# Performance work log

Hardware: AMD Instinct MI355X
Metric: run time of the kernel (lower is better)

The kernel has to match this reference:

```python
import jax, jax.numpy as jnp
import numpy as np
from jax import lax

N = 100000
E = 1600000
LAG = 50
H = 32          # hid_dim = in_channels = out_channels
FEA = 4
OUT = 1


def setup_inputs() -> dict:
    key = jax.random.key(0)
    ks = jax.random.split(key, 16)
    inp = {
        "node_x": jax.random.normal(ks[0], (N, FEA), jnp.float32),
        "node_yx": jax.random.normal(ks[1], (N, LAG), jnp.float32),
        "edge_index": jax.random.randint(ks[2], (2, E), 0, N, jnp.int64),
        "edge_weight": jax.random.uniform(ks[3], (E,), jnp.float32),
        # LSTM params (torch gate order: i, f, g, o)
        "w_ih": jax.random.normal(ks[4], (4 * H, 1), jnp.float32) * 0.1,
        "w_hh": jax.random.normal(ks[5], (4 * H, H), jnp.float32) * 0.1,
        "b_ih": jnp.zeros((4 * H,), jnp.float32),
        "b_hh": jnp.zeros((4 * H,), jnp.float32),
        # time attention
        "att_W": jax.random.normal(ks[6], (LAG, H), jnp.float32) * 0.1,
        # fc after attention pooling
        "fc_W": jax.random.normal(ks[7], (H, H), jnp.float32) * 0.1,
        "fc_b": jnp.zeros((H,), jnp.float32),
        # GCN layers
        "gcn1_W": jax.random.normal(ks[8], (H, H), jnp.float32) * 0.1,
        "gcn1_b": jnp.zeros((H,), jnp.float32),
        "gcn2_W": jax.random.normal(ks[9], (H, H), jnp.float32) * 0.1,
        "gcn2_b": jnp.zeros((H,), jnp.float32),
        # final linear
        "lin_W": jax.random.normal(ks[10], (H + FEA, OUT), jnp.float32) * 0.1,
        "lin_b": jnp.zeros((OUT,), jnp.float32),
    }
    return inp


def _lstm(x, w_ih, w_hh, b_ih, b_hh):
    # x: [N, T, in_dim]; returns ht: [N, T, H]
    n, t, _ = x.shape
    h = w_hh.shape[1]
    xp = jnp.einsum('nti,gi->ntg', x, w_ih) + b_ih  # [N,T,4H], precompute input proj
    xp = jnp.swapaxes(xp, 0, 1)                      # [T,N,4H]

    def step(carry, xt):
        hprev, cprev = carry
        g = xt + hprev @ w_hh.T + b_hh               # [N,4H]
        i = jax.nn.sigmoid(g[:, 0 * h:1 * h])
        f = jax.nn.sigmoid(g[:, 1 * h:2 * h])
        gg = jnp.tanh(g[:, 2 * h:3 * h])
        o = jax.nn.sigmoid(g[:, 3 * h:4 * h])
        c = f * cprev + i * gg
        hnew = o * jnp.tanh(c)
        return (hnew, c), hnew

    init = (jnp.zeros((n, h), x.dtype), jnp.zeros((n, h), x.dtype))
    _, hs = lax.scan(step, init, xp)
    return jnp.swapaxes(hs, 0, 1)                    # [N,T,H]


def _gcn(x, edge_index, edge_weight, W, b, num_nodes):
    # PyG GCNConv: x' = D^-1/2 (A + I) D^-1/2 (x W) + b
    xw = x @ W
    src = jnp.concatenate([edge_index[0], jnp.arange(num_nodes, dtype=edge_index.dtype)])
    dst = jnp.concatenate([edge_index[1], jnp.arange(num_nodes, dtype=edge_index.dtype)])
    ew = jnp.concatenate([edge_weight, jnp.ones((num_nodes,), edge_weight.dtype)])
    deg = jax.ops.segment_sum(ew, dst, num_segments=num_nodes)
    dis = jnp.where(deg > 0, deg ** -0.5, 0.0)
    norm = dis[src] * ew * dis[dst]                  # [E+N]
    msg = norm[:, None] * xw[src]                    # gather + scale
    out = jax.ops.segment_sum(msg, dst, num_segments=num_nodes)  # scatter-add
    return out + b


def reference(node_x, node_yx, edge_index, edge_weight,
              w_ih, w_hh, b_ih, b_hh, att_W, fc_W, fc_b,
              gcn1_W, gcn1_b, gcn2_W, gcn2_b, lin_W, lin_b):
    # ATT_LSTM
    ht = _lstm(node_yx[:, :, None], w_ih, w_hh, b_ih, b_hh)   # [N,LAG,H]
    scores = jnp.sum(ht * att_W, axis=2)                      # [N,LAG]
    att = jax.nn.softmax(scores, axis=1)
    pooled = jnp.einsum('nt,nth->nh', att, ht)                # [N,H]
    x1 = jax.nn.relu(pooled @ fc_W + fc_b)                    # [N,H]
    # dropout treated as identity (deterministic reference / eval mode)
    x2 = _gcn(x1, edge_index, edge_weight, gcn1_W, gcn1_b, N)
    x2 = _gcn(x2, edge_index, edge_weight, gcn2_W, gcn2_b, N)
    xcom = jnp.concatenate([x2, node_x], axis=1)              # [N,H+FEA]
    pred = jax.nn.relu(xcom @ lin_W + lin_b)                  # [N,1]
    return pred.squeeze(-1)                                   # [N]
```

## Files before the change

kernel.cpp:

```cpp
#include <hip/hip_runtime.h>
#include <hip/hip_bf16.h>
#include <stdint.h>
#include <math.h>

#define H 32
#define LAGN 50

typedef float f32x4 __attribute__((ext_vector_type(4)));
typedef short bf16x8 __attribute__((ext_vector_type(8)));

__device__ __forceinline__ float rcp_(float x){ return __builtin_amdgcn_rcpf(x); }
__device__ __forceinline__ float sigmoidf_(float x){ return rcp_(1.0f + __expf(-x)); }
__device__ __forceinline__ float tanhf_(float x){ return 1.0f - 2.0f*rcp_(__expf(2.0f*x) + 1.0f); }

__device__ __forceinline__ unsigned pk_bf2(float f0, float f1){
  union { __hip_bfloat162 b; unsigned u; } cv;
  cv.b = __float22bfloat162_rn(make_float2(f0, f1));
  return cv.u;
}
__device__ __forceinline__ void cvt8v(f32x4 a, f32x4 b, bf16x8& hi, bf16x8& lo){
  union U { bf16x8 v; unsigned d[4]; } Hu, Lu;
  #pragma unroll
  for (int p=0;p<2;p++){
    float f0=a[2*p], f1=a[2*p+1];
    unsigned uh = pk_bf2(f0,f1);
    float h0 = __uint_as_float(uh<<16);
    float h1 = __uint_as_float(uh & 0xffff0000u);
    Hu.d[p] = uh;  Lu.d[p] = pk_bf2(f0-h0, f1-h1);
    float g0=b[2*p], g1=b[2*p+1];
    unsigned ug = pk_bf2(g0,g1);
    float k0 = __uint_as_float(ug<<16);
    float k1 = __uint_as_float(ug & 0xffff0000u);
    Hu.d[2+p] = ug;  Lu.d[2+p] = pk_bf2(g0-k0, g1-k1);
  }
  hi = Hu.v; lo = Lu.v;
}

__global__ __launch_bounds__(256, 2) void k_lstm(
    const float* __restrict__ yx,
    const float* __restrict__ w_ih,
    const float* __restrict__ w_hh,
    const float* __restrict__ b_ih,
    const float* __restrict__ b_hh,
    const float* __restrict__ att_W,
    const float* __restrict__ fc_W,
    const float* __restrict__ fc_b,
    float* __restrict__ x1,
    int N)
{
  __shared__ float hs[4][16*36];
  const int wv = threadIdx.x >> 6;
  const int l  = threadIdx.x & 63;
  const int q  = l >> 4;
  const int cl = l & 15;
  const int nb = blockIdx.x*64 + wv*16;
  float* HS = hs[wv];

  bf16x8 Bhi[8], Blo[8];
  #pragma unroll
  for (int T=0; T<8; ++T){
    const float* p = w_hh + (size_t)(16*T + cl)*H + 8*q;
    f32x4 w0 = *(const f32x4*)p;
    f32x4 w1 = *(const f32x4*)(p+4);
    cvt8v(w0, w1, Bhi[T], Blo[T]);
  }

  float wihv[8], bsv[8];
  #pragma unroll
  for (int T=0;T<8;T++){
    int colg = 16*T + cl;
    wihv[T] = w_ih[colg];
    bsv[T]  = b_ih[colg] + b_hh[colg];
  }

  for (int i=l; i<16*36; i+=64) HS[i] = 0.f;

  float cst[4][2], Sv[4][2], Zv[4];
  #pragma unroll
  for (int idx=0;idx<4;idx++){
    Zv[idx]=0.f; cst[idx][0]=0.f; cst[idx][1]=0.f; Sv[idx][0]=0.f; Sv[idx][1]=0.f;
  }

  const int rr = nb + 4*q;
  const float* yp0 = yx + (size_t)(rr+0<N?rr+0:N-1)*LAGN;
  const float* yp1 = yx + (size_t)(rr+1<N?rr+1:N-1)*LAGN;
  const float* yp2 = yx + (size_t)(rr+2<N?rr+2:N-1)*LAGN;
  const float* yp3 = yx + (size_t)(rr+3<N?rr+3:N-1)*LAGN;

  #pragma unroll 1
  for (int t=0;t<LAGN;t++){
    float xtv[4] = {yp0[t], yp1[t], yp2[t], yp3[t]};
    float at0 = att_W[t*H + cl];
    float at1 = att_W[t*H + cl + 16];

    f32x4 a0 = *(const f32x4*)&HS[36*cl + 8*q];
    f32x4 a1 = *(const f32x4*)&HS[36*cl + 8*q + 4];
    bf16x8 Ahi, Alo;
    cvt8v(a0, a1, Ahi, Alo);

    f32x4 C[8];
    #pragma unroll
    for (int T=0;T<8;T++){
      f32x4 z;
      #pragma unroll
      for (int idx=0;idx<4;idx++) z[idx] = __builtin_fmaf(xtv[idx], wihv[T], bsv[T]);
      z = __builtin_amdgcn_mfma_f32_16x16x32_bf16(Ahi, Blo[T], z, 0,0,0);
      z = __builtin_amdgcn_mfma_f32_16x16x32_bf16(Alo, Bhi[T], z, 0,0,0);
      z = __builtin_amdgcn_mfma_f32_16x16x32_bf16(Ahi, Bhi[T], z, 0,0,0);
      C[T] = z;
    }

    float stp[4], hv[4][2];
    #pragma unroll
    for (int idx=0; idx<4; ++idx){
      stp[idx] = 0.f;
      #pragma unroll
      for (int jh=0; jh<2; ++jh){
        float iv = sigmoidf_(C[jh][idx]);
        float fv = sigmoidf_(C[2+jh][idx]);
        float gv = tanhf_(C[4+jh][idx]);
        float ov = sigmoidf_(C[6+jh][idx]);
        float cn = fv*cst[idx][jh] + iv*gv;
        cst[idx][jh] = cn;
        float hh = ov*tanhf_(cn);
        hv[idx][jh] = hh;
        stp[idx] += hh * (jh ? at1 : at0);
        HS[36*(4*q+idx) + cl + 16*jh] = hh;
      }
    }

    #pragma unroll
    for (int mask=1; mask<16; mask<<=1){
      #pragma unroll
      for (int idx=0;idx<4;idx++)
        stp[idx] += __shfl_xor(stp[idx], mask);
    }

    #pragma unroll
    for (int idx=0;idx<4;idx++){
      float pex = __expf(stp[idx]);
      Zv[idx] += pex;
      Sv[idx][0] += pex*hv[idx][0];
      Sv[idx][1] += pex*hv[idx][1];
    }
  }

  #pragma unroll
  for (int idx=0;idx<4;idx++){
    float iz = rcp_(Zv[idx]);
    HS[36*(4*q+idx) + cl]      = Sv[idx][0]*iz;
    HS[36*(4*q+idx) + cl + 16] = Sv[idx][1]*iz;
  }
  f32x4 p0 = *(const f32x4*)&HS[36*cl + 8*q];
  f32x4 p1 = *(const f32x4*)&HS[36*cl + 8*q + 4];
  bf16x8 Phi, Plo;
  cvt8v(p0, p1, Phi, Plo);

  #pragma unroll
  for (int T=0;T<2;T++){
    f32x4 w0, w1;
    #pragma unroll
    for (int i=0;i<4;i++){
      w0[i] = fc_W[(size_t)(8*q+i)*H + 16*T + cl];
      w1[i] = fc_W[(size_t)(8*q+4+i)*H + 16*T + cl];
    }
    bf16x8 Fhi, Flo;
    cvt8v(w0, w1, Fhi, Flo);
    float fcbv = fc_b[16*T + cl];
    f32x4 z = {fcbv, fcbv, fcbv, fcbv};
    z = __builtin_amdgcn_mfma_f32_16x16x32_bf16(Phi, Flo, z, 0,0,0);
    z = __builtin_amdgcn_mfma_f32_16x16x32_bf16(Plo, Fhi, z, 0,0,0);
    z = __builtin_amdgcn_mfma_f32_16x16x32_bf16(Phi, Fhi, z, 0,0,0);
    #pragma unroll
    for (int idx=0;idx<4;idx++){
      int r = nb + 4*q + idx;
      if (r < N) x1[(size_t)r*H + 16*T + cl] = fmaxf(z[idx], 0.f);
    }
  }
}

__global__ void k_deg_init(float* __restrict__ deg, int* __restrict__ cnt, int N){
  int i = blockIdx.x*blockDim.x + threadIdx.x;
  if (i < N){ deg[i] = 1.0f; cnt[i] = 0; }
}

__global__ void k_deg_cnt(const int* __restrict__ ei, const float* __restrict__ ew,
                          float* __restrict__ deg, int* __restrict__ cnt, int E){
  int e = blockIdx.x*blockDim.x + threadIdx.x;
  if (e < E){
    int d = ei[E+e];
    atomicAdd(&deg[d], ew[e]);
    atomicAdd(&cnt[d], 1);
  }
}

__global__ void k_dis(float* __restrict__ deg, int N){
  int i = blockIdx.x*blockDim.x + threadIdx.x;
  if (i < N) deg[i] = __frcp_rn(sqrtf(deg[i]));
}

__global__ __launch_bounds__(256) void k_scan1(const int* __restrict__ cnt,
                                               int* __restrict__ bsum, int N){
  __shared__ int wsm[4];
  int b = blockIdx.x, t = threadIdx.x;
  int base = b*1024 + t*4;
  int s = 0;
  #pragma unroll
  for (int i=0;i<4;i++) if (base+i < N) s += cnt[base+i];
  #pragma unroll
  for (int off=1; off<64; off<<=1) s += __shfl_xor(s, off);
  if ((t&63) == 0) wsm[t>>6] = s;
  __syncthreads();
  if (t == 0) bsum[b] = wsm[0]+wsm[1]+wsm[2]+wsm[3];
}

__global__ __launch_bounds__(64) void k_scan2(int* __restrict__ bsum, int nb){
  int lane = threadIdx.x;
  int carry = 0;
  for (int base=0; base<nb; base+=64){
    int i = base + lane;
    int v = (i<nb) ? bsum[i] : 0;
    int s = v;
    #pragma unroll
    for (int off=1; off<64; off<<=1){ int tt=__shfl_up(s,off); if (lane>=off) s+=tt; }
    if (i<nb) bsum[i] = carry + s - v;
    carry += __shfl(s, 63);
  }
}

__global__ __launch_bounds__(256) void k_scan3(int* cp,
                                               const int* __restrict__ bsum,
                                               int* __restrict__ rowptr, int N){
  __shared__ int wsm[4];
  int b = blockIdx.x, t = threadIdx.x, lane = t&63, w = t>>6;
  int base = b*1024 + t*4;
  int v[4];
  #pragma unroll
  for (int i=0;i<4;i++) v[i] = (base+i<N) ? cp[base+i] : 0;
  int tsum = v[0]+v[1]+v[2]+v[3];
  int s = tsum;
  #pragma unroll
  for (int off=1; off<64; off<<=1){ int tt=__shfl_up(s,off); if (lane>=off) s+=tt; }
  if (lane==63) wsm[w] = s;
  __syncthreads();
  int woff = 0;
  #pragma unroll
  for (int k=0;k<4;k++) if (k<w) woff += wsm[k];
  int e = bsum[b] + woff + (s - tsum);
  #pragma unroll
  for (int i=0;i<4;i++){
    if (base+i < N){ rowptr[base+i] = e; cp[base+i] = e; }
    if (base+i == N-1) rowptr[N] = e + v[i];
    e += v[i];
  }
}

__global__ void k_fill(const int* __restrict__ ei, const float* __restrict__ ew,
                       const float* __restrict__ dis, int* __restrict__ pos,
                       int2* __restrict__ cedge, int E){
  int e = blockIdx.x*blockDim.x + threadIdx.x;
  if (e < E){
    int s = ei[e], d = ei[E+e];
    int slot = atomicAdd(&pos[d], 1);
    cedge[slot] = make_int2(s, __float_as_int(dis[s]*ew[e]*dis[d]));
  }
}

__global__ __launch_bounds__(256) void k_xw(
    const float* __restrict__ x, const float* __restrict__ W,
    const float* __restrict__ b, const float* __restrict__ dis,
    float* __restrict__ xw, float* __restrict__ out, int N)
{
  int n = blockIdx.x*blockDim.x + threadIdx.x;
  if (n >= N) return;
  float xv[H];
  const float4* xr = (const float4*)(x + (size_t)n*H);
  #pragma unroll
  for (int q=0;q<H/4;q++){
    float4 v = xr[q];
    xv[4*q+0]=v.x; xv[4*q+1]=v.y; xv[4*q+2]=v.z; xv[4*q+3]=v.w;
  }
  float d = dis[n];
  float sn = d*d;
  float* xwr = xw + (size_t)n*H;
  float* outr = out + (size_t)n*H;
  #pragma unroll
  for (int j=0;j<H;j++){
    float a = 0.f;
    #pragma unroll
    for (int k=0;k<H;k++) a += xv[k]*W[k*H+j];
    xwr[j]  = a;
    outr[j] = sn*a + b[j];
  }
}

__global__ __launch_bounds__(256) void k_gather(
    const int* __restrict__ rowptr, const int2* __restrict__ cedge,
    const float* __restrict__ xw, float* __restrict__ out, int N)
{
  int wid = (int)((blockIdx.x*256u + threadIdx.x) >> 6);
  if (wid >= N) return;
  int lane = threadIdx.x & 63;
  int ch = lane & 31;
  int eh = lane >> 5;
  int start = rowptr[wid], end = rowptr[wid+1];
  float acc = 0.f;
  for (int j = start + eh; j < end; j += 2){
    int2 e = cedge[j];
    acc += __int_as_float(e.y) * xw[(size_t)e.x*H + ch];
  }
  acc += __shfl_xor(acc, 32);
  if (eh == 0){
    float* o = out + (size_t)wid*H + ch;
    *o += acc;
  }
}

__global__ void k_final(const float* __restrict__ x2, const float* __restrict__ nx,
                        const float* __restrict__ lw, const float* __restrict__ lb,
                        float* __restrict__ out, int N)
{
  int n = blockIdx.x*blockDim.x + threadIdx.x;
  if (n >= N) return;
  float a = lb[0];
  const float* xr = x2 + (size_t)n*H;
  #pragma unroll
  for (int j=0;j<H;j++) a += xr[j]*lw[j];
  const float* nr = nx + (size_t)n*4;
  #pragma unroll
  for (int f=0;f<4;f++) a += nr[f]*lw[H+f];
  out[n] = fmaxf(a, 0.f);
}

extern "C" void kernel_launch(void* const* d_in, const int* in_sizes, int n_in,
                              void* d_out, int out_size, void* d_ws, size_t ws_size,
                              hipStream_t stream) {
  const float* node_x   = (const float*)d_in[0];
  const float* node_yx  = (const float*)d_in[1];
  const int*   edge_idx = (const int*)  d_in[2];
  const float* edge_w   = (const float*)d_in[3];
  const float* w_ih     = (const float*)d_in[4];
  const float* w_hh     = (const float*)d_in[5];
  const float* b_ih     = (const float*)d_in[6];
  const float* b_hh     = (const float*)d_in[7];
  const float* att_W    = (const float*)d_in[8];
  const float* fc_W     = (const float*)d_in[9];
  const float* fc_b     = (const float*)d_in[10];
  const float* gcn1_W   = (const float*)d_in[11];
  const float* gcn1_b   = (const float*)d_in[12];
  const float* gcn2_W   = (const float*)d_in[13];
  const float* gcn2_b   = (const float*)d_in[14];
  const float* lin_W    = (const float*)d_in[15];
  const float* lin_b    = (const float*)d_in[16];
  float* out = (float*)d_out;

  int N = in_sizes[0] / 4;
  int E = in_sizes[3];

  float* ws = (float*)d_ws;
  float* x1     = ws;
  float* xw     = x1  + (size_t)N*H;
  float* o1     = xw  + (size_t)N*H;
  float* deg    = o1  + (size_t)N*H;
  int*   rowptr = (int*)(deg + N);
  int*   pos    = rowptr + (N+1);
  uintptr_t ca  = ((uintptr_t)(pos + N) + 7) & ~(uintptr_t)7;
  int2*  cedge  = (int2*)ca;
  int*   bsum   = (int*)(cedge + E);

  dim3 blk(256);
  int gN  = (N + 255) / 256;
  int gE  = (E + 255) / 256;
  int gL  = (N + 63) / 64;
  int gG  = (N + 3) / 4;
  int gS  = (N + 1023) / 1024;

  k_lstm<<<gL, blk, 0, stream>>>(node_yx, w_ih, w_hh, b_ih, b_hh,
                                 att_W, fc_W, fc_b, x1, N);
  k_deg_init<<<gN, blk, 0, stream>>>(deg, pos, N);
  k_deg_cnt <<<gE, blk, 0, stream>>>(edge_idx, edge_w, deg, pos, E);
  k_dis     <<<gN, blk, 0, stream>>>(deg, N);
  k_scan1   <<<gS, blk, 0, stream>>>(pos, bsum, N);
  k_scan2   <<<1, dim3(64), 0, stream>>>(bsum, gS);
  k_scan3   <<<gS, blk, 0, stream>>>(pos, bsum, rowptr, N);
  k_fill    <<<gE, blk, 0, stream>>>(edge_idx, edge_w, deg, pos, cedge, E);
  k_xw    <<<gN, blk, 0, stream>>>(x1, gcn1_W, gcn1_b, deg, xw, o1, N);
  k_gather<<<gG, blk, 0, stream>>>(rowptr, cedge, xw, o1, N);
  k_xw    <<<gN, blk, 0, stream>>>(o1, gcn2_W, gcn2_b, deg, xw, x1, N);
  k_gather<<<gG, blk, 0, stream>>>(rowptr, cedge, xw, x1, N);
  k_final<<<gN, blk, 0, stream>>>(x1, node_x, lin_W, lin_b, out, N);
}
```

Baseline: 772.9 us.

## Interleave two independent node tiles per wave in the LSTM kernel

```diff
diff --git a/kernel.cpp b/kernel.cpp
--- a/kernel.cpp
+++ b/kernel.cpp
@@ -36,6 +36,55 @@
   hi = Hu.v; lo = Lu.v;
 }
 
+struct C8 { f32x4 v[8]; };
+
+__device__ __forceinline__ C8 tile_mfma(
+    const float* HS, const bf16x8 (&Bhi)[8], const bf16x8 (&Blo)[8],
+    const float (&wihv)[8], const float (&bsv)[8], const float (&xtv)[4],
+    int q, int cl)
+{
+  f32x4 a0 = *(const f32x4*)&HS[36*cl + 8*q];
+  f32x4 a1 = *(const f32x4*)&HS[36*cl + 8*q + 4];
+  bf16x8 Ahi, Alo;
+  cvt8v(a0, a1, Ahi, Alo);
+  C8 C;
+  #pragma unroll
+  for (int T=0;T<8;T++){
+    f32x4 z;
+    #pragma unroll
+    for (int idx=0;idx<4;idx++) z[idx] = __builtin_fmaf(xtv[idx], wihv[T], bsv[T]);
+    z = __builtin_amdgcn_mfma_f32_16x16x32_bf16(Ahi, Blo[T], z, 0,0,0);
+    z = __builtin_amdgcn_mfma_f32_16x16x32_bf16(Alo, Bhi[T], z, 0,0,0);
+    z = __builtin_amdgcn_mfma_f32_16x16x32_bf16(Ahi, Bhi[T], z, 0,0,0);
+    C.v[T] = z;
+  }
+  return C;
+}
+
+__device__ __forceinline__ void tile_gates(
+    float* HS, const C8& C, float at0, float at1,
+    float (&cst)[4][2], float (&hv)[4][2], float (&stp)[4],
+    int q, int cl)
+{
+  #pragma unroll
+  for (int idx=0; idx<4; ++idx){
+    stp[idx] = 0.f;
+    #pragma unroll
+    for (int jh=0; jh<2; ++jh){
+      float iv = sigmoidf_(C.v[jh][idx]);
+      float fv = sigmoidf_(C.v[2+jh][idx]);
+      float gv = tanhf_(C.v[4+jh][idx]);
+      float ov = sigmoidf_(C.v[6+jh][idx]);
+      float cn = fv*cst[idx][jh] + iv*gv;
+      cst[idx][jh] = cn;
+      float hh = ov*tanhf_(cn);
+      hv[idx][jh] = hh;
+      stp[idx] += hh * (jh ? at1 : at0);
+      HS[36*(4*q+idx) + cl + 16*jh] = hh;
+    }
+  }
+}
+
 __global__ __launch_bounds__(256, 2) void k_lstm(
     const float* __restrict__ yx,
     const float* __restrict__ w_ih,
@@ -48,13 +97,15 @@
     float* __restrict__ x1,
     int N)
 {
-  __shared__ float hs[4][16*36];
+  __shared__ float hs[8][16*36];
   const int wv = threadIdx.x >> 6;
   const int l  = threadIdx.x & 63;
   const int q  = l >> 4;
   const int cl = l & 15;
-  const int nb = blockIdx.x*64 + wv*16;
-  float* HS = hs[wv];
+  const int nbA = blockIdx.x*128 + wv*32;
+  const int nbB = nbA + 16;
+  float* HSA = hs[2*wv];
+  float* HSB = hs[2*wv+1];
 
   bf16x8 Bhi[8], Blo[8];
   #pragma unroll
@@ -73,108 +124,98 @@
     bsv[T]  = b_ih[colg] + b_hh[colg];
   }
 
-  for (int i=l; i<16*36; i+=64) HS[i] = 0.f;
-
-  float cst[4][2], Sv[4][2], Zv[4];
+  for (int i=l; i<16*36; i+=64){ HSA[i] = 0.f; HSB[i] = 0.f; }
+
+  float cstA[4][2], SvA[4][2], ZvA[4];
+  float cstB[4][2], SvB[4][2], ZvB[4];
   #pragma unroll
   for (int idx=0;idx<4;idx++){
-    Zv[idx]=0.f; cst[idx][0]=0.f; cst[idx][1]=0.f; Sv[idx][0]=0.f; Sv[idx][1]=0.f;
-  }
-
-  const int rr = nb + 4*q;
-  const float* yp0 = yx + (size_t)(rr+0<N?rr+0:N-1)*LAGN;
-  const float* yp1 = yx + (size_t)(rr+1<N?rr+1:N-1)*LAGN;
-  const float* yp2 = yx + (size_t)(rr+2<N?rr+2:N-1)*LAGN;
-  const float* yp3 = yx + (size_t)(rr+3<N?rr+3:N-1)*LAGN;
+    ZvA[idx]=0.f; ZvB[idx]=0.f;
+    #pragma unroll
+    for (int jh=0;jh<2;jh++){ cstA[idx][jh]=0.f; SvA[idx][jh]=0.f;
+                              cstB[idx][jh]=0.f; SvB[idx][jh]=0.f; }
+  }
+
+  const int rrA = nbA + 4*q, rrB = nbB + 4*q;
+  const int rcA = (rrA <= N-4) ? rrA : (N>=4 ? N-4 : 0);
+  const int rcB = (rrB <= N-4) ? rrB : (N>=4 ? N-4 : 0);
+  const float* yA = yx + (size_t)rcA*LAGN;
+  const float* yB = yx + (size_t)rcB*LAGN;
 
   #pragma unroll 1
   for (int t=0;t<LAGN;t++){
-    float xtv[4] = {yp0[t], yp1[t], yp2[t], yp3[t]};
     float at0 = att_W[t*H + cl];
     float at1 = att_W[t*H + cl + 16];
-
-    f32x4 a0 = *(const f32x4*)&HS[36*cl + 8*q];
-    f32x4 a1 = *(const f32x4*)&HS[36*cl + 8*q + 4];
-    bf16x8 Ahi, Alo;
-    cvt8v(a0, a1, Ahi, Alo);
-
-    f32x4 C[8];
-    #pragma unroll
-    for (int T=0;T<8;T++){
-      f32x4 z;
+    float xtA[4] = {yA[t], yA[t+LAGN], yA[t+2*LAGN], yA[t+3*LAGN]};
+    float xtB[4] = {yB[t], yB[t+LAGN], yB[t+2*LAGN], yB[t+3*LAGN]};
+
+    C8 CA = tile_mfma(HSA, Bhi, Blo, wihv, bsv, xtA, q, cl);
+    C8 CB = tile_mfma(HSB, Bhi, Blo, wihv, bsv, xtB, q, cl);
+
+    float hvA[4][2], stpA[4], hvB[4][2], stpB[4];
+    tile_gates(HSA, CA, at0, at1, cstA, hvA, stpA, q, cl);
+    tile_gates(HSB, CB, at0, at1, cstB, hvB, stpB, q, cl);
+
+    #pragma unroll
+    for (int mask=1; mask<16; mask<<=1){
       #pragma unroll
-      for (int idx=0;idx<4;idx++) z[idx] = __builtin_fmaf(xtv[idx], wihv[T], bsv[T]);
-      z = __builtin_amdgcn_mfma_f32_16x16x32_bf16(Ahi, Blo[T], z, 0,0,0);
-      z = __builtin_amdgcn_mfma_f32_16x16x32_bf16(Alo, Bhi[T], z, 0,0,0);
-      z = __builtin_amdgcn_mfma_f32_16x16x32_bf16(Ahi, Bhi[T], z, 0,0,0);
-      C[T] = z;
-    }
-
-    float stp[4], hv[4][2];
-    #pragma unroll
-    for (int idx=0; idx<4; ++idx){
-      stp[idx] = 0.f;
-      #pragma unroll
-      for (int jh=0; jh<2; ++jh){
-        float iv = sigmoidf_(C[jh][idx]);
-        float fv = sigmoidf_(C[2+jh][idx]);
-        float gv = tanhf_(C[4+jh][idx]);
-        float ov = sigmoidf_(C[6+jh][idx]);
-        float cn = fv*cst[idx][jh] + iv*gv;
-        cst[idx][jh] = cn;
-        float hh = ov*tanhf_(cn);
-        hv[idx][jh] = hh;
-        stp[idx] += hh * (jh ? at1 : at0);
-        HS[36*(4*q+idx) + cl + 16*jh] = hh;
+      for (int idx=0;idx<4;idx++){
+        stpA[idx] += __shfl_xor(stpA[idx], mask);
+        stpB[idx] += __shfl_xor(stpB[idx], mask);
       }
     }
 
     #pragma unroll
-    for (int mask=1; mask<16; mask<<=1){
+    for (int idx=0;idx<4;idx++){
+      float pA = __expf(stpA[idx]);
+      ZvA[idx] += pA;
+      SvA[idx][0] += pA*hvA[idx][0];
+      SvA[idx][1] += pA*hvA[idx][1];
+      float pB = __expf(stpB[idx]);
+      ZvB[idx] += pB;
+      SvB[idx][0] += pB*hvB[idx][0];
+      SvB[idx][1] += pB*hvB[idx][1];
+    }
+  }
+
+  #pragma unroll
+  for (int idx=0;idx<4;idx++){
+    float izA = rcp_(ZvA[idx]);
+    HSA[36*(4*q+idx) + cl]      = SvA[idx][0]*izA;
+    HSA[36*(4*q+idx) + cl + 16] = SvA[idx][1]*izA;
+    float izB = rcp_(ZvB[idx]);
+    HSB[36*(4*q+idx) + cl]      = SvB[idx][0]*izB;
+    HSB[36*(4*q+idx) + cl + 16] = SvB[idx][1]*izB;
+  }
+
+  #pragma unroll
+  for (int tb=0; tb<2; ++tb){
+    float* HS = tb ? HSB : HSA;
+    int nb = tb ? nbB : nbA;
+    f32x4 p0 = *(const f32x4*)&HS[36*cl + 8*q];
+    f32x4 p1 = *(const f32x4*)&HS[36*cl + 8*q + 4];
+    bf16x8 Phi, Plo;
+    cvt8v(p0, p1, Phi, Plo);
+    #pragma unroll
+    for (int T=0;T<2;T++){
+      f32x4 w0, w1;
       #pragma unroll
-      for (int idx=0;idx<4;idx++)
-        stp[idx] += __shfl_xor(stp[idx], mask);
-    }
-
-    #pragma unroll
-    for (int idx=0;idx<4;idx++){
-      float pex = __expf(stp[idx]);
-      Zv[idx] += pex;
-      Sv[idx][0] += pex*hv[idx][0];
-      Sv[idx][1] += pex*hv[idx][1];
-    }
-  }
-
-  #pragma unroll
-  for (int idx=0;idx<4;idx++){
-    float iz = rcp_(Zv[idx]);
-    HS[36*(4*q+idx) + cl]      = Sv[idx][0]*iz;
-    HS[36*(4*q+idx) + cl + 16] = Sv[idx][1]*iz;
-  }
-  f32x4 p0 = *(const f32x4*)&HS[36*cl + 8*q];
-  f32x4 p1 = *(const f32x4*)&HS[36*cl + 8*q + 4];
-  bf16x8 Phi, Plo;
-  cvt8v(p0, p1, Phi, Plo);
-
-  #pragma unroll
-  for (int T=0;T<2;T++){
-    f32x4 w0, w1;
-    #pragma unroll
-    for (int i=0;i<4;i++){
-      w0[i] = fc_W[(size_t)(8*q+i)*H + 16*T + cl];
-      w1[i] = fc_W[(size_t)(8*q+4+i)*H + 16*T + cl];
-    }
-    bf16x8 Fhi, Flo;
-    cvt8v(w0, w1, Fhi, Flo);
-    float fcbv = fc_b[16*T + cl];
-    f32x4 z = {fcbv, fcbv, fcbv, fcbv};
-    z = __builtin_amdgcn_mfma_f32_16x16x32_bf16(Phi, Flo, z, 0,0,0);
-    z = __builtin_amdgcn_mfma_f32_16x16x32_bf16(Plo, Fhi, z, 0,0,0);
-    z = __builtin_amdgcn_mfma_f32_16x16x32_bf16(Phi, Fhi, z, 0,0,0);
-    #pragma unroll
-    for (int idx=0;idx<4;idx++){
-      int r = nb + 4*q + idx;
-      if (r < N) x1[(size_t)r*H + 16*T + cl] = fmaxf(z[idx], 0.f);
+      for (int i=0;i<4;i++){
+        w0[i] = fc_W[(size_t)(8*q+i)*H + 16*T + cl];
+        w1[i] = fc_W[(size_t)(8*q+4+i)*H + 16*T + cl];
+      }
+      bf16x8 Fhi, Flo;
+      cvt8v(w0, w1, Fhi, Flo);
+      float fcbv = fc_b[16*T + cl];
+      f32x4 z = {fcbv, fcbv, fcbv, fcbv};
+      z = __builtin_amdgcn_mfma_f32_16x16x32_bf16(Phi, Flo, z, 0,0,0);
+      z = __builtin_amdgcn_mfma_f32_16x16x32_bf16(Plo, Fhi, z, 0,0,0);
+      z = __builtin_amdgcn_mfma_f32_16x16x32_bf16(Phi, Fhi, z, 0,0,0);
+      #pragma unroll
+      for (int idx=0;idx<4;idx++){
+        int r = nb + 4*q + idx;
+        if (r < N) x1[(size_t)r*H + 16*T + cl] = fmaxf(z[idx], 0.f);
+      }
     }
   }
 }
@@ -371,7 +412,7 @@
   dim3 blk(256);
   int gN  = (N + 255) / 256;
   int gE  = (E + 255) / 256;
-  int gL  = (N + 63) / 64;
+  int gL  = (N + 127) / 128;
   int gG  = (N + 3) / 4;
   int gS  = (N + 1023) / 1024;
 
```

New measurement: 833.8 us. 1.08x slower.
